# Performance work log

Measured on AMD Instinct MI355X. Metric: run time of the kernel, lower is better.

## Reference

```python
import jax, jax.numpy as jnp
import numpy as np

# --- dims / hyperparams (match init_kwargs) ---
B, W, D = 2048, 6, 1024
H, R = 8, 64
DH = D // H            # per-head dim = 128
DT = 0.09
COUPLING = 0.01
TOL = 0.05
THIGH = 0.22
MAX_STEPS = 16


def setup_inputs() -> dict:
    key = jax.random.key(0)
    k1, k2, k3, k4 = jax.random.split(key, 4)
    S = jax.random.normal(k1, (B, W, D), jnp.float32)
    signal = jax.random.normal(k2, (B, W, D), jnp.float32) * 0.01
    # low-rank per-head diffusion factors, scaled for stable Euler steps
    U = jax.random.normal(k3, (H, DH, R), jnp.float32) * 0.05
    V = jax.random.normal(k4, (H, R, DH), jnp.float32) * 0.05
    return {"S": S, "signal": signal, "U": U, "V": V}


def _tension(S):
    # geometry-only tension: 1 - mean cosine to mean direction, shape (B,)
    normed = S / (jnp.linalg.norm(S, axis=-1, keepdims=True) + 1e-12)
    mean_dir = normed.mean(axis=1)                        # (B, D)
    cos = jnp.einsum('bwd,bd->bw', normed, mean_dir)      # (B, W)
    return 1.0 - cos.mean(axis=-1)


def _dynamics(S, signal, U, V):
    noise_key = jax.random.key(1)

    def drift(x):  # x: (B, W, D)
        xh = x.reshape(B, W, H, DH)
        # per-head low-rank diffusion: -(x_h U_h) V_h
        diff = -jnp.einsum('bwhd,hdr,hre->bwhe', xh, U, V)
        # hierarchical cross-head alignment coupling
        mean_h = xh.mean(axis=2, keepdims=True)
        out = diff + COUPLING * (mean_h - xh)
        return out.reshape(B, W, D) + signal

    def clamp_norm(x):
        n = jnp.linalg.norm(x, axis=-1, keepdims=True)
        return x * (jnp.clip(n, 1e-3, 12.0) / jnp.maximum(n, 1e-8))

    def step(carry, k):
        Sc, done = carry
        Sn = clamp_norm(Sc + DT * drift(Sc))               # one Euler step
        T = _tension(Sn)                                   # (B,)
        new_done = done | jnp.all(T < TOL)                 # early-exit (break)
        # tension-too-high branch: noise kick + renormalize to unit sphere
        noise = 0.01 * jax.random.normal(jax.random.fold_in(noise_key, k), Sn.shape, Sn.dtype)
        Sz = Sn + noise
        Sz = Sz / (jnp.linalg.norm(Sz, axis=-1, keepdims=True) + 1e-8)
        apply_noise = (~new_done) & jnp.any(T > THIGH)
        Snext = jnp.where(apply_noise, Sz, Sn)
        Sout = jnp.where(done, Sc, Snext)                  # frozen after break
        t_rec = jnp.where(done, jnp.nan, T.mean())
        return (Sout, new_done), t_rec

    (Sf, _), curve = jax.lax.scan(step, (S, jnp.array(False)), jnp.arange(MAX_STEPS))
    return Sf, curve


def reference(S, signal, U, V):
    return _dynamics(S, signal, U, V)
```

## Files before the change

### kernel.cpp

```cpp
#include <hip/hip_runtime.h>
#include <stdint.h>

#define NB 2048
#define NW 6
#define ND 1024
#define NH 8
#define NDH 128
#define NDP 1028
#define NTOT 12582912u
#define BT 256
#define C_DT 0.09f
#define C_COUP 0.01f
#define C_TOL 0.05f
#define C_THIGH 0.22f
#define NSTEPS 16

typedef __attribute__((ext_vector_type(8))) short short8v;
typedef __attribute__((ext_vector_type(4))) float f32x4;

struct Flags {
  int done; int apply_noise;
};

__host__ __device__ __forceinline__ uint32_t rotl32(uint32_t x, uint32_t d) {
  return (x << d) | (x >> (32u - d));
}

__host__ __device__ __forceinline__ void tf2x32(uint32_t k0, uint32_t k1,
                                                uint32_t x0, uint32_t x1,
                                                uint32_t& o0, uint32_t& o1) {
  const uint32_t k2 = k0 ^ k1 ^ 0x1BD11BDAu;
#define TF_R4(a,b,c,d) \
  x0 += x1; x1 = rotl32(x1,a); x1 ^= x0; \
  x0 += x1; x1 = rotl32(x1,b); x1 ^= x0; \
  x0 += x1; x1 = rotl32(x1,c); x1 ^= x0; \
  x0 += x1; x1 = rotl32(x1,d); x1 ^= x0;
  x0 += k0; x1 += k1;
  TF_R4(13u,15u,26u,6u)  x0 += k1; x1 += k2 + 1u;
  TF_R4(17u,29u,16u,24u) x0 += k2; x1 += k0 + 2u;
  TF_R4(13u,15u,26u,6u)  x0 += k0; x1 += k1 + 3u;
  TF_R4(17u,29u,16u,24u) x0 += k1; x1 += k2 + 4u;
  TF_R4(13u,15u,26u,6u)  x0 += k2; x1 += k0 + 5u;
#undef TF_R4
  o0 = x0; o1 = x1;
}

__device__ __forceinline__ float erfinv_fast(float x) {
  const float w = -__logf(fmaf(x, -x, 1.0f));
  const float ws = w - 2.5f;
  float ps = 2.81022636e-08f;
  ps = fmaf(ps, ws, 3.43273939e-07f);
  ps = fmaf(ps, ws, -3.5233877e-06f);
  ps = fmaf(ps, ws, -4.39150654e-06f);
  ps = fmaf(ps, ws, 0.00021858087f);
  ps = fmaf(ps, ws, -0.00125372503f);
  ps = fmaf(ps, ws, -0.00417768164f);
  ps = fmaf(ps, ws, 0.246640727f);
  ps = fmaf(ps, ws, 1.50140941f);
  if (__any(w >= 5.0f)) {
    const float wb = sqrtf(w) - 3.0f;
    float pb = -0.000200214257f;
    pb = fmaf(pb, wb, 0.000100950558f);
    pb = fmaf(pb, wb, 0.00134934322f);
    pb = fmaf(pb, wb, -0.00367342844f);
    pb = fmaf(pb, wb, 0.00573950773f);
    pb = fmaf(pb, wb, -0.0076224613f);
    pb = fmaf(pb, wb, 0.00943887047f);
    pb = fmaf(pb, wb, 1.00167406f);
    pb = fmaf(pb, wb, 2.83297682f);
    return ((w < 5.0f) ? ps : pb) * x;
  }
  return ps * x;
}

__device__ __forceinline__ float noise_z(uint32_t k0, uint32_t k1, uint32_t p) {
  uint32_t o0, o1;
  tf2x32(k0, k1, 0u, p, o0, o1);
  const uint32_t bits = o0 ^ o1;
  const float f = __uint_as_float((bits >> 9) | 0x3F800000u) - 1.0f;
  const float lo = -0.99999994f;
  const float u = fmaxf(lo, fmaf(f, 2.0f, lo));
  return 1.41421356237f * erfinv_fast(u);
}

__device__ __forceinline__ unsigned short f2bf(float f) {
  const uint32_t u = __float_as_uint(f);
  return (unsigned short)((u + 0x7FFFu + ((u >> 16) & 1u)) >> 16);
}

__device__ __forceinline__ void block_sum6(float p[NW], float* red ) {
  #pragma unroll
  for (int w = 0; w < NW; ++w)
    #pragma unroll
    for (int off = 32; off > 0; off >>= 1) p[w] += __shfl_down(p[w], off, 64);
  const int t = threadIdx.x;
  __syncthreads();
  if ((t & 63) == 0) {
    #pragma unroll
    for (int w = 0; w < NW; ++w) red[(t >> 6) * NW + w] = p[w];
  }
  __syncthreads();
  #pragma unroll
  for (int w = 0; w < NW; ++w)
    p[w] = red[w] + red[NW + w] + red[2 * NW + w] + red[3 * NW + w];
}

__device__ __forceinline__ float block_sum4(float v, float* red) {
  #pragma unroll
  for (int off = 32; off > 0; off >>= 1) v += __shfl_down(v, off, 64);
  const int t = threadIdx.x;
  __syncthreads();
  if ((t & 63) == 0) red[t >> 6] = v;
  __syncthreads();
  return red[0] + red[1] + red[2] + red[3];
}

__global__ void init_kernel(Flags* f, float* curve) {
  const int t = threadIdx.x;
  if (t == 0) { f->done = 0; f->apply_noise = 0; }
  if (t < NSTEPS) curve[t] = __int_as_float(0x7FC00000);
}

__global__ __launch_bounds__(128) void precompute_M(const float* __restrict__ U,
                                                    const float* __restrict__ V,
                                                    unsigned short* __restrict__ Mhi) {
  const int hd = blockIdx.x;
  const int h = hd >> 7;
  const int d = hd & 127;
  const int e = threadIdx.x;
  __shared__ float u[64];
  if (e < 64) u[e] = U[hd * 64 + e];
  __syncthreads();
  float acc = 0.0f;
  #pragma unroll
  for (int r = 0; r < 64; ++r)
    acc = fmaf(u[r], V[(h * 64 + r) * 128 + e], acc);
  const int nt = e >> 4, ks = d >> 5;
  const int lane = (e & 15) | (((d >> 3) & 3) << 4);
  const int j = d & 7;
  const size_t idx = ((((size_t)(h * 8 + nt)) * 4 + ks) * 64 + lane) * 8 + j;
  Mhi[idx] = f2bf(acc);
}

__global__ __launch_bounds__(BT, 4) void step_kernel(
    const float* __restrict__ Sin, float* __restrict__ Sout,
    const float* __restrict__ signal,
    const unsigned short* __restrict__ Mhi,
    const Flags* __restrict__ flags, float* __restrict__ Tarr,
    const uint32_t nk0, const uint32_t nk1, const int has_noise) {
  if (flags->done) return;
  __shared__ __align__(16) float xs[NW][NDP];
  __shared__ __align__(16) float mh[NW][NDH];
  __shared__ float red[4 * NW];
  const int t = threadIdx.x;
  const int b = blockIdx.x;
  const int e0 = t << 2;

  float v[NW][4];
  float sg[NW][4];
  #pragma unroll
  for (int w = 0; w < NW; ++w) {
    const float4 a = *reinterpret_cast<const float4*>(
        Sin + (size_t)(b * NW + w) * ND + e0);
    v[w][0]=a.x; v[w][1]=a.y; v[w][2]=a.z; v[w][3]=a.w;
  }
  #pragma unroll
  for (int w = 0; w < NW; ++w) {
    const float4 a = *reinterpret_cast<const float4*>(
        signal + (size_t)(b * NW + w) * ND + e0);
    sg[w][0]=a.x; sg[w][1]=a.y; sg[w][2]=a.z; sg[w][3]=a.w;
  }
  if (has_noise && flags->apply_noise) {
    float p[NW];
    #pragma unroll
    for (int w = 0; w < NW; ++w) {
      const uint32_t rowbase = (uint32_t)(b * NW + w) * ND + (uint32_t)e0;
      #pragma unroll
      for (int j = 0; j < 4; ++j)
        v[w][j] = fmaf(0.01f, noise_z(nk0, nk1, rowbase + (uint32_t)j), v[w][j]);
      p[w] = v[w][0]*v[w][0] + v[w][1]*v[w][1] + v[w][2]*v[w][2] + v[w][3]*v[w][3];
    }
    block_sum6(p, red);
    #pragma unroll
    for (int w = 0; w < NW; ++w) {
      const float inv = 1.0f / (sqrtf(p[w]) + 1e-8f);
      #pragma unroll
      for (int j = 0; j < 4; ++j) v[w][j] *= inv;
    }
  }
  #pragma unroll
  for (int w = 0; w < NW; ++w) {
    float4 a; a.x=v[w][0]; a.y=v[w][1]; a.z=v[w][2]; a.w=v[w][3];
    *reinterpret_cast<float4*>(&xs[w][e0]) = a;
  }
  __syncthreads();

  for (int idx = t; idx < NW * NDH; idx += BT) {
    const int w = idx >> 7, el = idx & 127;
    float s = 0.0f;
    #pragma unroll
    for (int hh = 0; hh < NH; ++hh) s += xs[w][hh * NDH + el];
    mh[w][el] = s * 0.125f;
  }
  __syncthreads();

  {
    const int l = t & 63, wv = t >> 6;
    const int arow = l & 15, kg = l >> 4;
    #pragma unroll 1
    for (int h2 = 0; h2 < 2; ++h2) {
      const int hh = wv * 2 + h2;
      f32x4 acc0,acc1,acc2,acc3,acc4,acc5,acc6,acc7;
      acc0=acc1=acc2=acc3=acc4=acc5=acc6=acc7=(f32x4){0.f,0.f,0.f,0.f};
      f32x4* accp[8] = {&acc0,&acc1,&acc2,&acc3,&acc4,&acc5,&acc6,&acc7};
      #pragma unroll
      for (int ks = 0; ks < 4; ++ks) {
        short8v ahi = (short8v)0;
        if (arow < NW) {
          const float* xp = &xs[arow][hh * NDH + ks * 32 + kg * 8];
          const float4 xa = *reinterpret_cast<const float4*>(xp);
          const float4 xb = *reinterpret_cast<const float4*>(xp + 4);
          const float xf[8] = {xa.x,xa.y,xa.z,xa.w,xb.x,xb.y,xb.z,xb.w};
          #pragma unroll
          for (int j = 0; j < 8; ++j) ahi[j] = (short)f2bf(xf[j]);
        }
        #pragma unroll
        for (int nt = 0; nt < 8; ++nt) {
          const size_t fo = ((((size_t)(hh * 8 + nt)) * 4 + ks) * 64 + l) * 8;
          const short8v bhi = *reinterpret_cast<const short8v*>(Mhi + fo);
          *accp[nt] = __builtin_amdgcn_mfma_f32_16x16x32_bf16(ahi, bhi, *accp[nt], 0, 0, 0);
        }
      }
      #pragma unroll
      for (int nt = 0; nt < 8; ++nt) {
        const f32x4 a = *accp[nt];
        #pragma unroll
        for (int r = 0; r < 4; ++r) {
          const int row = kg * 4 + r;
          if (row < NW) xs[row][hh * NDH + nt * 16 + arow] = a[r];
        }
      }
    }
  }
  __syncthreads();

  float acc[NW][4];
  float p[NW];
  #pragma unroll
  for (int w = 0; w < NW; ++w) {
    const float4 dv = *reinterpret_cast<const float4*>(&xs[w][e0]);
    const float4 hh = *reinterpret_cast<const float4*>(&mh[w][e0 & 127]);
    const float dvf[4] = {dv.x, dv.y, dv.z, dv.w};
    const float mhf[4] = {hh.x, hh.y, hh.z, hh.w};
    float s2 = 0.0f;
    #pragma unroll
    for (int j = 0; j < 4; ++j) {
      const float out = -dvf[j] + C_COUP * (mhf[j] - v[w][j]) + sg[w][j];
      acc[w][j] = fmaf(C_DT, out, v[w][j]);
      s2 = fmaf(acc[w][j], acc[w][j], s2);
    }
    p[w] = s2;
  }

  block_sum6(p, red);
  #pragma unroll
  for (int w = 0; w < NW; ++w) {
    const float n = sqrtf(p[w]);
    const float scale = fminf(fmaxf(n, 1e-3f), 12.0f) / fmaxf(n, 1e-8f);
    const float inv_norm = 1.0f / (n * scale + 1e-12f);
    float4 o;
    o.x = acc[w][0]*scale; o.y = acc[w][1]*scale;
    o.z = acc[w][2]*scale; o.w = acc[w][3]*scale;
    *reinterpret_cast<float4*>(Sout + (size_t)(b * NW + w) * ND + e0) = o;
    acc[w][0]=o.x*inv_norm; acc[w][1]=o.y*inv_norm;
    acc[w][2]=o.z*inv_norm; acc[w][3]=o.w*inv_norm;
  }

  float pc[NW];
  #pragma unroll
  for (int w = 0; w < NW; ++w) pc[w] = 0.0f;
  #pragma unroll
  for (int j = 0; j < 4; ++j) {
    float md = 0.0f;
    #pragma unroll
    for (int w = 0; w < NW; ++w) md += acc[w][j];
    md *= (1.0f / 6.0f);
    #pragma unroll
    for (int w = 0; w < NW; ++w) pc[w] = fmaf(acc[w][j], md, pc[w]);
  }
  block_sum6(pc, red);

  if (t == 0) {
    const float cos_sum = pc[0]+pc[1]+pc[2]+pc[3]+pc[4]+pc[5];
    Tarr[b] = 1.0f - cos_sum * (1.0f / 6.0f);
  }
}

__global__ __launch_bounds__(256) void flags_kernel(
    Flags* __restrict__ f, const float* __restrict__ Tarr,
    float* __restrict__ curve, const int step_k) {
  __shared__ float red[12];
  const int t = threadIdx.x;
  const int done_old = f->done;
  float s = 0.0f, cl = 0.0f, ch = 0.0f;
  for (int i = t; i < NB; i += 256) {
    const float T = Tarr[i];
    s += T;
    cl += (T < C_TOL) ? 1.0f : 0.0f;
    ch += (T > C_THIGH) ? 1.0f : 0.0f;
  }
  #pragma unroll
  for (int off = 32; off > 0; off >>= 1) {
    s  += __shfl_down(s,  off, 64);
    cl += __shfl_down(cl, off, 64);
    ch += __shfl_down(ch, off, 64);
  }
  if ((t & 63) == 0) {
    red[(t >> 6) * 3 + 0] = s;
    red[(t >> 6) * 3 + 1] = cl;
    red[(t >> 6) * 3 + 2] = ch;
  }
  __syncthreads();
  if (t == 0) {
    const float sT  = red[0] + red[3] + red[6] + red[9];
    const float cln = red[1] + red[4] + red[7] + red[10];
    const float chn = red[2] + red[5] + red[8] + red[11];
    curve[step_k] = done_old ? __int_as_float(0x7FC00000) : sT * (1.0f / 2048.0f);
    const int nd = (done_old || cln == (float)NB) ? 1 : 0;
    f->apply_noise = (!nd && chn > 0.0f) ? 1 : 0;
    f->done = nd;
  }
}

__global__ __launch_bounds__(256) void noise_kernel(float* __restrict__ S,
                                                    const Flags* __restrict__ flags,
                                                    const uint32_t k0, const uint32_t k1) {
  if (!flags->apply_noise) return;
  __shared__ float red[4];
  const int t = threadIdx.x;
  const uint32_t base = (uint32_t)blockIdx.x * ND + (t << 2);
  const float4 s = *reinterpret_cast<const float4*>(S + base);
  float v[4] = {s.x, s.y, s.z, s.w};
  #pragma unroll
  for (int j = 0; j < 4; ++j)
    v[j] = fmaf(0.01f, noise_z(k0, k1, base + (uint32_t)j), v[j]);
  const float p2 = v[0]*v[0] + v[1]*v[1] + v[2]*v[2] + v[3]*v[3];
  const float n2 = block_sum4(p2, red);
  const float inv = 1.0f / (sqrtf(n2) + 1e-8f);
  float4 o;
  o.x = v[0]*inv; o.y = v[1]*inv; o.z = v[2]*inv; o.w = v[3]*inv;
  *reinterpret_cast<float4*>(S + base) = o;
}

extern "C" void kernel_launch(void* const* d_in, const int* in_sizes, int n_in,
                              void* d_out, int out_size, void* d_ws, size_t ws_size,
                              hipStream_t stream) {
  const float* S0     = (const float*)d_in[0];
  const float* signal = (const float*)d_in[1];
  const float* U      = (const float*)d_in[2];
  const float* V      = (const float*)d_in[3];
  float* out   = (float*)d_out;
  float* curve = out + NTOT;
  Flags* flags = (Flags*)d_ws;
  float* Tarr  = (float*)((char*)d_ws + 512);
  unsigned short* Mhi = (unsigned short*)((char*)d_ws + 16384);

  init_kernel<<<1, 32, 0, stream>>>(flags, curve);
  precompute_M<<<NH * NDH, 128, 0, stream>>>(U, V, Mhi);

  uint32_t K0[NSTEPS], K1[NSTEPS];
  for (uint32_t k = 0; k < NSTEPS; ++k) tf2x32(0u, 1u, 0u, k, K0[k], K1[k]);

  for (int k = 0; k < NSTEPS; ++k) {
    step_kernel<<<NB, BT, 0, stream>>>(
        k == 0 ? S0 : out, out, signal, Mhi, flags, Tarr,
        k > 0 ? K0[k - 1] : 0u, k > 0 ? K1[k - 1] : 0u, k > 0 ? 1 : 0);
    flags_kernel<<<1, 256, 0, stream>>>(flags, Tarr, curve, k);
  }
  noise_kernel<<<NB * NW, 256, 0, stream>>>(out, flags, K0[NSTEPS - 1], K1[NSTEPS - 1]);
}
```

Baseline: 1.094 ms.

## Fuse flag reduction into step kernel and store shared activations as bf16

```diff
diff --git a/kernel.cpp b/kernel.cpp
--- a/kernel.cpp
+++ b/kernel.cpp
@@ -6,7 +6,7 @@
 #define ND 1024
 #define NH 8
 #define NDH 128
-#define NDP 1028
+#define NSP 1032
 #define NTOT 12582912u
 #define BT 256
 #define C_DT 0.09f
@@ -18,9 +18,7 @@
 typedef __attribute__((ext_vector_type(8))) short short8v;
 typedef __attribute__((ext_vector_type(4))) float f32x4;
 
-struct Flags {
-  int done; int apply_noise;
-};
+struct Flags { int apply_noise; };
 
 __host__ __device__ __forceinline__ uint32_t rotl32(uint32_t x, uint32_t d) {
   return (x << d) | (x >> (32u - d));
@@ -87,6 +85,9 @@
   const uint32_t u = __float_as_uint(f);
   return (unsigned short)((u + 0x7FFFu + ((u >> 16) & 1u)) >> 16);
 }
+__device__ __forceinline__ float bf2f(unsigned short h) {
+  return __uint_as_float(((uint32_t)h) << 16);
+}
 
 __device__ __forceinline__ void block_sum6(float p[NW], float* red ) {
   #pragma unroll
@@ -115,10 +116,13 @@
   return red[0] + red[1] + red[2] + red[3];
 }
 
-__global__ void init_kernel(Flags* f, float* curve) {
-  const int t = threadIdx.x;
-  if (t == 0) { f->done = 0; f->apply_noise = 0; }
-  if (t < NSTEPS) curve[t] = __int_as_float(0x7FC00000);
+__global__ void init_kernel(Flags* f, int* doneArr, float* curve) {
+  const int t = threadIdx.x;
+  if (t == 0) f->apply_noise = 0;
+  if (t < NSTEPS) {
+    doneArr[t] = 0;
+    curve[t] = __int_as_float(0x7FC00000);
+  }
 }
 
 __global__ __launch_bounds__(128) void precompute_M(const float* __restrict__ U,
@@ -142,16 +146,18 @@
   Mhi[idx] = f2bf(acc);
 }
 
-__global__ __launch_bounds__(BT, 4) void step_kernel(
+__global__ __launch_bounds__(BT, 8) void step_kernel(
     const float* __restrict__ Sin, float* __restrict__ Sout,
     const float* __restrict__ signal,
     const unsigned short* __restrict__ Mhi,
-    const Flags* __restrict__ flags, float* __restrict__ Tarr,
-    const uint32_t nk0, const uint32_t nk1, const int has_noise) {
-  if (flags->done) return;
-  __shared__ __align__(16) float xs[NW][NDP];
+    float* __restrict__ Tarr, int* __restrict__ doneArr,
+    float* __restrict__ curve,
+    const int step_k, const uint32_t nk0, const uint32_t nk1) {
+  __shared__ __align__(16) unsigned short xs[NW][NSP];
   __shared__ __align__(16) float mh[NW][NDH];
   __shared__ float red[4 * NW];
+  __shared__ int   redI[8];
+  __shared__ float redF[4];
   const int t = threadIdx.x;
   const int b = blockIdx.x;
   const int e0 = t << 2;
@@ -170,7 +176,45 @@
         signal + (size_t)(b * NW + w) * ND + e0);
     sg[w][0]=a.x; sg[w][1]=a.y; sg[w][2]=a.z; sg[w][3]=a.w;
   }
-  if (has_noise && flags->apply_noise) {
+
+  int apply = 0;
+  if (step_k > 0) {
+    const float* Tprev = Tarr + (size_t)((step_k - 1) & 1) * NB;
+    bool aL = true, aH = false;
+    float s = 0.0f;
+    #pragma unroll
+    for (int i = 0; i < NB / BT; ++i) {
+      const float T = Tprev[i * BT + t];
+      aL = aL && (T < C_TOL);
+      aH = aH || (T > C_THIGH);
+      s += T;
+    }
+    #pragma unroll
+    for (int off = 32; off > 0; off >>= 1) s += __shfl_down(s, off, 64);
+    const int wAll = __all(aL) ? 1 : 0;
+    const int wAny = __any(aH) ? 1 : 0;
+    if ((t & 63) == 0) {
+      redI[(t >> 6) * 2 + 0] = wAll;
+      redI[(t >> 6) * 2 + 1] = wAny;
+      redF[t >> 6] = s;
+    }
+    __syncthreads();
+    const int allLow  = redI[0] & redI[2] & redI[4] & redI[6];
+    const int anyHigh = redI[1] | redI[3] | redI[5] | redI[7];
+    const int dprev2 = doneArr[step_k - 1];
+    const int d1 = dprev2 | allLow;
+    apply = (!d1 && anyHigh) ? 1 : 0;
+    if (b == 0 && t == 0) {
+      doneArr[step_k] = d1;
+      if (!dprev2) {
+        const float sT = redF[0] + redF[1] + redF[2] + redF[3];
+        curve[step_k - 1] = sT * (1.0f / 2048.0f);
+      }
+    }
+    if (d1) return;
+  }
+
+  if (apply) {
     float p[NW];
     #pragma unroll
     for (int w = 0; w < NW; ++w) {
@@ -190,8 +234,9 @@
   }
   #pragma unroll
   for (int w = 0; w < NW; ++w) {
-    float4 a; a.x=v[w][0]; a.y=v[w][1]; a.z=v[w][2]; a.w=v[w][3];
-    *reinterpret_cast<float4*>(&xs[w][e0]) = a;
+    const uint32_t p0 = (uint32_t)f2bf(v[w][0]) | ((uint32_t)f2bf(v[w][1]) << 16);
+    const uint32_t p1 = (uint32_t)f2bf(v[w][2]) | ((uint32_t)f2bf(v[w][3]) << 16);
+    *reinterpret_cast<uint2*>(&xs[w][e0]) = make_uint2(p0, p1);
   }
   __syncthreads();
 
@@ -199,7 +244,7 @@
     const int w = idx >> 7, el = idx & 127;
     float s = 0.0f;
     #pragma unroll
-    for (int hh = 0; hh < NH; ++hh) s += xs[w][hh * NDH + el];
+    for (int hh = 0; hh < NH; ++hh) s += bf2f(xs[w][hh * NDH + el]);
     mh[w][el] = s * 0.125f;
   }
   __syncthreads();
@@ -216,14 +261,9 @@
       #pragma unroll
       for (int ks = 0; ks < 4; ++ks) {
         short8v ahi = (short8v)0;
-        if (arow < NW) {
-          const float* xp = &xs[arow][hh * NDH + ks * 32 + kg * 8];
-          const float4 xa = *reinterpret_cast<const float4*>(xp);
-          const float4 xb = *reinterpret_cast<const float4*>(xp + 4);
-          const float xf[8] = {xa.x,xa.y,xa.z,xa.w,xb.x,xb.y,xb.z,xb.w};
-          #pragma unroll
-          for (int j = 0; j < 8; ++j) ahi[j] = (short)f2bf(xf[j]);
-        }
+        if (arow < NW)
+          ahi = *reinterpret_cast<const short8v*>(
+              &xs[arow][hh * NDH + ks * 32 + kg * 8]);
         #pragma unroll
         for (int nt = 0; nt < 8; ++nt) {
           const size_t fo = ((((size_t)(hh * 8 + nt)) * 4 + ks) * 64 + l) * 8;
@@ -237,7 +277,7 @@
         #pragma unroll
         for (int r = 0; r < 4; ++r) {
           const int row = kg * 4 + r;
-          if (row < NW) xs[row][hh * NDH + nt * 16 + arow] = a[r];
+          if (row < NW) xs[row][hh * NDH + nt * 16 + arow] = f2bf(a[r]);
         }
       }
     }
@@ -248,9 +288,11 @@
   float p[NW];
   #pragma unroll
   for (int w = 0; w < NW; ++w) {
-    const float4 dv = *reinterpret_cast<const float4*>(&xs[w][e0]);
+    const uint2 d2 = *reinterpret_cast<const uint2*>(&xs[w][e0]);
     const float4 hh = *reinterpret_cast<const float4*>(&mh[w][e0 & 127]);
-    const float dvf[4] = {dv.x, dv.y, dv.z, dv.w};
+    const float dvf[4] = {
+        bf2f((unsigned short)(d2.x & 0xFFFFu)), bf2f((unsigned short)(d2.x >> 16)),
+        bf2f((unsigned short)(d2.y & 0xFFFFu)), bf2f((unsigned short)(d2.y >> 16))};
     const float mhf[4] = {hh.x, hh.y, hh.z, hh.w};
     float s2 = 0.0f;
     #pragma unroll
@@ -292,43 +334,40 @@
 
   if (t == 0) {
     const float cos_sum = pc[0]+pc[1]+pc[2]+pc[3]+pc[4]+pc[5];
-    Tarr[b] = 1.0f - cos_sum * (1.0f / 6.0f);
-  }
-}
-
-__global__ __launch_bounds__(256) void flags_kernel(
-    Flags* __restrict__ f, const float* __restrict__ Tarr,
-    float* __restrict__ curve, const int step_k) {
-  __shared__ float red[12];
-  const int t = threadIdx.x;
-  const int done_old = f->done;
-  float s = 0.0f, cl = 0.0f, ch = 0.0f;
+    Tarr[(size_t)(step_k & 1) * NB + b] = 1.0f - cos_sum * (1.0f / 6.0f);
+  }
+}
+
+__global__ __launch_bounds__(256) void flags_final(
+    Flags* __restrict__ f, const float* __restrict__ Tprev,
+    const int* __restrict__ doneArr, float* __restrict__ curve) {
+  __shared__ int redI[8];
+  __shared__ float redF[4];
+  const int t = threadIdx.x;
+  bool aL = true, aH = false;
+  float s = 0.0f;
   for (int i = t; i < NB; i += 256) {
-    const float T = Tarr[i];
+    const float T = Tprev[i];
+    aL = aL && (T < C_TOL);
+    aH = aH || (T > C_THIGH);
     s += T;
-    cl += (T < C_TOL) ? 1.0f : 0.0f;
-    ch += (T > C_THIGH) ? 1.0f : 0.0f;
-  }
-  #pragma unroll
-  for (int off = 32; off > 0; off >>= 1) {
-    s  += __shfl_down(s,  off, 64);
-    cl += __shfl_down(cl, off, 64);
-    ch += __shfl_down(ch, off, 64);
-  }
+  }
+  #pragma unroll
+  for (int off = 32; off > 0; off >>= 1) s += __shfl_down(s, off, 64);
   if ((t & 63) == 0) {
-    red[(t >> 6) * 3 + 0] = s;
-    red[(t >> 6) * 3 + 1] = cl;
-    red[(t >> 6) * 3 + 2] = ch;
+    redI[(t >> 6) * 2 + 0] = __all(aL) ? 1 : 0;
+    redI[(t >> 6) * 2 + 1] = __any(aH) ? 1 : 0;
+    redF[t >> 6] = s;
   }
   __syncthreads();
   if (t == 0) {
-    const float sT  = red[0] + red[3] + red[6] + red[9];
-    const float cln = red[1] + red[4] + red[7] + red[10];
-    const float chn = red[2] + red[5] + red[8] + red[11];
-    curve[step_k] = done_old ? __int_as_float(0x7FC00000) : sT * (1.0f / 2048.0f);
-    const int nd = (done_old || cln == (float)NB) ? 1 : 0;
-    f->apply_noise = (!nd && chn > 0.0f) ? 1 : 0;
-    f->done = nd;
+    const int allLow  = redI[0] & redI[2] & redI[4] & redI[6];
+    const int anyHigh = redI[1] | redI[3] | redI[5] | redI[7];
+    const int dprev = doneArr[NSTEPS - 1];
+    if (!dprev)
+      curve[NSTEPS - 1] = (redF[0]+redF[1]+redF[2]+redF[3]) * (1.0f / 2048.0f);
+    const int dfin = dprev | allLow;
+    f->apply_noise = (!dfin && anyHigh) ? 1 : 0;
   }
 }
 
@@ -361,11 +400,12 @@
   const float* V      = (const float*)d_in[3];
   float* out   = (float*)d_out;
   float* curve = out + NTOT;
-  Flags* flags = (Flags*)d_ws;
-  float* Tarr  = (float*)((char*)d_ws + 512);
-  unsigned short* Mhi = (unsigned short*)((char*)d_ws + 16384);
-
-  init_kernel<<<1, 32, 0, stream>>>(flags, curve);
+  Flags* flags   = (Flags*)d_ws;
+  int*   doneArr = (int*)((char*)d_ws + 64);
+  float* Tarr    = (float*)((char*)d_ws + 1024);
+  unsigned short* Mhi = (unsigned short*)((char*)d_ws + 32768);
+
+  init_kernel<<<1, 32, 0, stream>>>(flags, doneArr, curve);
   precompute_M<<<NH * NDH, 128, 0, stream>>>(U, V, Mhi);
 
   uint32_t K0[NSTEPS], K1[NSTEPS];
@@ -373,9 +413,9 @@
 
   for (int k = 0; k < NSTEPS; ++k) {
     step_kernel<<<NB, BT, 0, stream>>>(
-        k == 0 ? S0 : out, out, signal, Mhi, flags, Tarr,
-        k > 0 ? K0[k - 1] : 0u, k > 0 ? K1[k - 1] : 0u, k > 0 ? 1 : 0);
-    flags_kernel<<<1, 256, 0, stream>>>(flags, Tarr, curve, k);
-  }
+        k == 0 ? S0 : out, out, signal, Mhi, Tarr, doneArr, curve, k,
+        k > 0 ? K0[k - 1] : 0u, k > 0 ? K1[k - 1] : 0u);
+  }
+  flags_final<<<1, 256, 0, stream>>>(flags, Tarr + NB, doneArr, curve);
   noise_kernel<<<NB * NW, 256, 0, stream>>>(out, flags, K0[NSTEPS - 1], K1[NSTEPS - 1]);
 }
```

New measurement: 1.509 ms. 37.9% more time.
